# Kernel tuning notes

Hardware: AMD Instinct MI355X
Metric: run time of the kernel (lower is better)

## Reference

```python
import jax, jax.numpy as jnp
import numpy as np

UNITS = 1024
LEVELS = 16
CHUNK = UNITS // LEVELS  # 64


def cumsoftmax(x, mode):
    # softmax then cumsum along last axis; 'r2l' reverses before/after
    if mode == 'l2r':
        return jnp.cumsum(jax.nn.softmax(x, axis=-1), axis=-1)
    else:  # 'r2l'
        xr = x[..., ::-1]
        return jnp.cumsum(jax.nn.softmax(xr, axis=-1), axis=-1)[..., ::-1]


def setup_inputs() -> dict:
    key = jax.random.key(0)
    k1, k2, k3 = jax.random.split(key, 3)
    B, T, D = 32, 512, 1024
    G = UNITS * 4 + LEVELS * 2  # 4128
    x = jax.random.normal(k1, (B, T, D), dtype=jnp.float32)
    kernel = jax.random.normal(k2, (D, G), dtype=jnp.float32) * (1.0 / np.sqrt(D))
    recurrent_kernel = jax.random.normal(k3, (UNITS, G), dtype=jnp.float32) * (1.0 / np.sqrt(UNITS))
    bias = jnp.zeros((G,), dtype=jnp.float32)
    return {"x": x, "kernel": kernel, "recurrent_kernel": recurrent_kernel, "bias": bias}


def reference(x, kernel, recurrent_kernel, bias):
    B, T, D = x.shape
    L, U, C = LEVELS, UNITS, CHUNK

    def one_step(carry, x_t):
        c_last, h_last = carry  # [B, U] each
        z = x_t @ kernel + h_last @ recurrent_kernel + bias  # [B, 4U+2L]
        f_master = cumsoftmax(z[:, :L], 'l2r')[:, :, None]       # [B, L, 1]
        i_master = cumsoftmax(z[:, L:2 * L], 'r2l')[:, :, None]  # [B, L, 1]
        g = z[:, 2 * L:].reshape(B, 4 * L, C)
        f_gate = jax.nn.sigmoid(g[:, :L])
        i_gate = jax.nn.sigmoid(g[:, L:2 * L])
        o_gate = jax.nn.sigmoid(g[:, 2 * L:3 * L])
        c_in = jnp.tanh(g[:, 3 * L:])
        c_prev = c_last.reshape(B, L, C)
        overlap = f_master * i_master
        c_out = (overlap * (f_gate * c_prev + i_gate * c_in)
                 + (f_master - overlap) * c_prev
                 + (i_master - overlap) * c_in)
        h_out = (o_gate * jnp.tanh(c_out)).reshape(B, U)
        c_out = c_out.reshape(B, U)
        return (c_out, h_out), h_out

    init = (jnp.zeros((B, U), x.dtype), jnp.zeros((B, U), x.dtype))
    _, h_seq = jax.lax.scan(one_step, init, jnp.swapaxes(x, 0, 1))  # [T, B, U]
    return jnp.swapaxes(h_seq, 0, 1)  # [B, T, U] (return_sequences=True)
```

## Files before the change

### kernel.cpp

```cpp
#include <hip/hip_runtime.h>

#define TT 512
#define GG 4128
#define GPAD 4224
#define NGATE 64
#define NMST 4
#define NBLK (NGATE + NMST)
#define NTHR 512

typedef _Float16 f16;
typedef _Float16 half8 __attribute__((ext_vector_type(8)));
typedef _Float16 half4 __attribute__((ext_vector_type(4)));
typedef float f32x4 __attribute__((ext_vector_type(4)));
typedef unsigned long long ull;

__device__ __forceinline__ half8 h8(uint4 v) {
  union { uint4 u; half8 h; } c; c.u = v; return c.h;
}

__global__ void k_transpose_cvt(const float* __restrict__ in, f16* __restrict__ out,
                                int R, int C) {
  __shared__ float tile[32][33];
  int bx = blockIdx.x * 32, by = blockIdx.y * 32;
  int tx = threadIdx.x & 31, ty = threadIdx.x >> 5;
#pragma unroll
  for (int j = 0; j < 4; ++j) {
    int r = by + ty + j * 8;
    tile[ty + j * 8][tx] = in[(long)r * C + bx + tx];
  }
  __syncthreads();
#pragma unroll
  for (int j = 0; j < 4; ++j) {
    int c = bx + ty + j * 8;
    out[(long)c * R + by + tx] = (f16)tile[tx][ty + j * 8];
  }
}

__global__ __launch_bounds__(256) void k_gemm_xw(
    const float* __restrict__ X,
    const f16* __restrict__ Bt,
    const float* __restrict__ bias,
    f16* __restrict__ Zm,
    f16* __restrict__ Zg) {
  __shared__ f16 As[128 * 32];
  __shared__ f16 Bs[128 * 32];
  const int m0 = blockIdx.x * 128;
  const int n0 = blockIdx.y * 128;
  const int tid = threadIdx.x;
  const int wave = tid >> 6, lane = tid & 63;
  const int mrow = (wave & 1) * 64, ncol = (wave >> 1) * 64;
  f32x4 acc[4][4];
#pragma unroll
  for (int i = 0; i < 4; ++i)
#pragma unroll
    for (int j = 0; j < 4; ++j)
      acc[i][j] = (f32x4){0.f, 0.f, 0.f, 0.f};

  float4 ra[4];
  uint4 rb[2];
  auto load_tiles = [&](int k0) {
#pragma unroll
    for (int q = 0; q < 4; ++q) {
      int flat = q * 256 + tid;
      int r = flat >> 3, s = flat & 7;
      ra[q] = *(const float4*)(X + (long)(m0 + r) * 1024 + k0 + s * 4);
    }
#pragma unroll
    for (int q = 0; q < 2; ++q) {
      int flat = q * 256 + tid;
      int r = flat >> 2, s = flat & 3;
      rb[q] = *(const uint4*)(Bt + (long)(n0 + r) * 1024 + k0 + s * 8);
    }
  };
  load_tiles(0);
  for (int kt = 0; kt < 32; ++kt) {
    __syncthreads();
#pragma unroll
    for (int q = 0; q < 4; ++q) {
      int flat = q * 256 + tid;
      half4 h;
      h[0] = (f16)ra[q].x; h[1] = (f16)ra[q].y;
      h[2] = (f16)ra[q].z; h[3] = (f16)ra[q].w;
      *(half4*)((char*)As + flat * 8) = h;
    }
#pragma unroll
    for (int q = 0; q < 2; ++q) {
      int flat = q * 256 + tid;
      *(uint4*)((char*)Bs + flat * 16) = rb[q];
    }
    __syncthreads();
    if (kt + 1 < 32) load_tiles((kt + 1) * 32);
    const int kseg2 = ((lane >> 4) * 8) * 2;
    half8 af[4], bf[4];
#pragma unroll
    for (int i = 0; i < 4; ++i) {
      int r = mrow + i * 16 + (lane & 15);
      af[i] = *(const half8*)((const char*)As + r * 64 + kseg2);
      int c = ncol + i * 16 + (lane & 15);
      bf[i] = *(const half8*)((const char*)Bs + c * 64 + kseg2);
    }
#pragma unroll
    for (int i = 0; i < 4; ++i)
#pragma unroll
      for (int j = 0; j < 4; ++j)
        acc[i][j] = __builtin_amdgcn_mfma_f32_16x16x32_f16(af[i], bf[j], acc[i][j], 0, 0, 0);
  }
#pragma unroll
  for (int j = 0; j < 4; ++j) {
    int n = n0 + ncol + j * 16 + (lane & 15);
    if (n < GG) {
      float bv = bias[n];
      const int isM = (n < 32);
      int q = 0, u4 = 0, g2 = 0;
      if (!isM) {
        int k = n - 32;
        q = k >> 10;
        int u = k & 1023;
        g2 = u >> 4;
        u4 = u & 15;
      }
#pragma unroll
      for (int i = 0; i < 4; ++i) {
#pragma unroll
        for (int r = 0; r < 4; ++r) {
          int m = m0 + mrow + i * 16 + (lane >> 4) * 4 + r;
          int b = m >> 9, tt2 = m & 511;
          f16 v = (f16)(acc[i][j][r] + bv);
          if (isM)
            Zm[((long)(tt2 * 32 + b)) * 32 + n] = v;
          else
            Zg[((((long)tt2 * 64 + g2) * 32 + b) * 16 + u4) * 4 + q] = v;
        }
      }
    }
  }
}

__device__ __forceinline__ float sigm(float x) { return 1.f / (1.f + __expf(-x)); }
__device__ __forceinline__ float tanh_(float x) {
  float ax = fabsf(x);
  float e = __expf(-2.f * ax);
  float t = (1.f - e) / (1.f + e);
  return copysignf(t, x);
}
#define AG_LD(p) __hip_atomic_load((p), __ATOMIC_RELAXED, __HIP_MEMORY_SCOPE_AGENT)
#define AG_ST(p, v) __hip_atomic_store((p), (v), __ATOMIC_RELAXED, __HIP_MEMORY_SCOPE_AGENT)

__device__ __forceinline__ void bar_lds() {
  asm volatile("s_waitcnt lgkmcnt(0)" ::: "memory");
  __builtin_amdgcn_sched_barrier(0);
  __builtin_amdgcn_s_barrier();
}

__global__ __launch_bounds__(NTHR, 2) void k_onlstm(
    const f16* __restrict__ Zm, const f16* __restrict__ Zg,
    const f16* __restrict__ Rt, unsigned* __restrict__ hbuf,
    float* __restrict__ cumbuf, unsigned* __restrict__ flags,
    unsigned* __restrict__ mflags, float* __restrict__ Y) {
  extern __shared__ char lds[];
  const int g = blockIdx.x, tid = threadIdx.x;
  const int wave = tid >> 6, lane = tid & 63;
  const int lr = lane & 15, lq = lane >> 4;

  if (g < NGATE) {
    const int kq = wave;
    const int b = tid >> 4;
    const int u = tid & 15;
    const int L0 = g >> 2;
    uint4 bq[16];
    {
      const f16* base = Rt + (long)kq * 128 + lq * 8;
#pragma unroll
      for (int q = 0; q < 4; ++q)
#pragma unroll
        for (int ks = 0; ks < 4; ++ks)
          bq[q * 4 + ks] = *(const uint4*)(base + (long)(32 + q * 1024 + g * 16 + lr) * 1024 + ks * 32);
#pragma unroll
      for (int i = 0; i < 16; ++i)
        asm volatile("" : "+v"(bq[i].x), "+v"(bq[i].y), "+v"(bq[i].z), "+v"(bq[i].w));
    }
    float creg = 0.f;

    for (int t = 0; t < TT; ++t) {
      if (t > 0) {
        for (;;) {
          unsigned v = AG_LD(flags + lane * 16);
          if (__all((int)(v >= (unsigned)t))) break;
        }
      }
      half4 zxh = *(const half4*)(Zg + ((((long)t * 64 + g) * 32 + b) * 16 + u) * 4);
      const ull* hrd = (const ull*)hbuf + (t & 1) * 8192;
      ull hv[16];
#pragma unroll
      for (int it = 0; it < 16; ++it)
        hv[it] = AG_LD(hrd + it * 512 + tid);
      __builtin_amdgcn_sched_barrier(0);
#pragma unroll
      for (int it = 0; it < 16; ++it) {
        int idx = it * 512 + tid;
        int bb = idx >> 8, j8 = idx & 255;
        *(ull*)(lds + ((bb * 128 + ((j8 >> 1) ^ (bb & 7))) << 4) + (j8 & 1) * 8) = hv[it];
      }
      bar_lds();
      f32x4 acc[4][2];
#pragma unroll
      for (int q = 0; q < 4; ++q) {
        acc[q][0] = (f32x4){0.f, 0.f, 0.f, 0.f};
        acc[q][1] = (f32x4){0.f, 0.f, 0.f, 0.f};
      }
#pragma unroll
      for (int ks = 0; ks < 4; ++ks) {
        int ch = kq * 16 + ks * 4 + lq;
        half8 a0 = *(const half8*)(lds + ((lr * 128 + (ch ^ (lr & 7))) << 4));
        half8 a1 = *(const half8*)(lds + (((16 + lr) * 128 + (ch ^ ((16 + lr) & 7))) << 4));
#pragma unroll
        for (int q = 0; q < 4; ++q) {
          acc[q][0] = __builtin_amdgcn_mfma_f32_16x16x32_f16(a0, h8(bq[q * 4 + ks]), acc[q][0], 0, 0, 0);
          acc[q][1] = __builtin_amdgcn_mfma_f32_16x16x32_f16(a1, h8(bq[q * 4 + ks]), acc[q][1], 0, 0, 0);
        }
      }
#pragma unroll
      for (int q = 0; q < 4; ++q)
#pragma unroll
        for (int bt = 0; bt < 2; ++bt) {
          int bsw = (bt * 16 + lq * 4) ^ ((lr & 7) << 2);
          *(f32x4*)(lds + 65536 + (((kq * 64 + q * 16 + lr) * 32 + bsw) << 2)) = acc[q][bt];
        }
      bar_lds();
      for (;;) {
        unsigned v = AG_LD(mflags + (lane & 3) * 16);
        if (__all((int)(v >= (unsigned)(t + 1)))) break;
      }
      unsigned fmu = AG_LD((unsigned*)cumbuf + b * 32 + L0);
      unsigned imu = AG_LD((unsigned*)cumbuf + b * 32 + 16 + L0);
      float z[4];
#pragma unroll
      for (int q = 0; q < 4; ++q) {
        float s = 0.f;
        int bsw = b ^ ((u & 7) << 2);
#pragma unroll
        for (int k8 = 0; k8 < 8; ++k8)
          s += *(const float*)(lds + 65536 + (((k8 * 64 + q * 16 + u) * 32 + bsw) << 2));
        z[q] = s + (float)zxh[q];
      }
      float f = sigm(z[0]), i_ = sigm(z[1]), o = sigm(z[2]);
      float ci = tanh_(z[3]);
      float fm = __uint_as_float(fmu), im = __uint_as_float(imu);
      float ov = fm * im;
      float cn = ov * (f * creg + i_ * ci) + (fm - ov) * creg + (im - ov) * ci;
      creg = cn;
      float hval = o * tanh_(cn);
      float hp = __shfl_xor(hval, 1);
      if (!(u & 1)) {
        union { f16 h[2]; unsigned w; } pk;
        pk.h[0] = (f16)hval;
        pk.h[1] = (f16)hp;
        AG_ST(hbuf + ((t + 1) & 1) * 16384 + b * 512 + g * 8 + (u >> 1), pk.w);
      }
      asm volatile("s_waitcnt vmcnt(0)" ::: "memory");
      __builtin_amdgcn_s_barrier();
      if (tid == 0) AG_ST(flags + g * 16, (unsigned)(t + 1));
      Y[((long)b * TT + t) * 1024 + g * 16 + u] = hval;
    }
  } else {
    const int mid = g - NGATE;
    const int ct = wave & 1, kq4 = wave >> 1;
    const int colm = ct * 16 + lr;
    uint4 bm[8];
    {
      const f16* pm = Rt + (long)colm * 1024 + kq4 * 256 + lq * 8;
#pragma unroll
      for (int ks = 0; ks < 8; ++ks) bm[ks] = *(const uint4*)(pm + ks * 32);
#pragma unroll
      for (int i = 0; i < 8; ++i)
        asm volatile("" : "+v"(bm[i].x), "+v"(bm[i].y), "+v"(bm[i].z), "+v"(bm[i].w));
    }
    const int rb_ = tid & 31, rc = tid >> 5;
    const int sb = tid >> 4, sl = tid & 15;
    float* zpm = (float*)(lds + 65536);
    float* zr = (float*)(lds + 65536 + 16384);

    for (int t = 0; t < TT; ++t) {
      if (t > 0) {
        for (;;) {
          unsigned v = AG_LD(flags + lane * 16);
          if (__all((int)(v >= (unsigned)t))) break;
        }
      }
      f16 zm0 = Zm[((long)t * 32 + rb_) * 32 + rc];
      f16 zm1 = Zm[((long)t * 32 + rb_) * 32 + rc + 16];
      const ull* hrd = (const ull*)hbuf + (t & 1) * 8192;
      ull hv[16];
#pragma unroll
      for (int it = 0; it < 16; ++it)
        hv[it] = AG_LD(hrd + it * 512 + tid);
      __builtin_amdgcn_sched_barrier(0);
#pragma unroll
      for (int it = 0; it < 16; ++it) {
        int idx = it * 512 + tid;
        int bb = idx >> 8, j8 = idx & 255;
        *(ull*)(lds + ((bb * 128 + ((j8 >> 1) ^ (bb & 7))) << 4) + (j8 & 1) * 8) = hv[it];
      }
      bar_lds();
      f32x4 am0 = (f32x4){0.f, 0.f, 0.f, 0.f}, am1 = am0;
#pragma unroll
      for (int ks = 0; ks < 8; ++ks) {
        int ch = kq4 * 32 + ks * 4 + lq;
        half8 a0 = *(const half8*)(lds + ((lr * 128 + (ch ^ (lr & 7))) << 4));
        half8 a1 = *(const half8*)(lds + (((16 + lr) * 128 + (ch ^ ((16 + lr) & 7))) << 4));
        am0 = __builtin_amdgcn_mfma_f32_16x16x32_f16(a0, h8(bm[ks]), am0, 0, 0, 0);
        am1 = __builtin_amdgcn_mfma_f32_16x16x32_f16(a1, h8(bm[ks]), am1, 0, 0, 0);
      }
      {
        int bsw0 = (lq * 4) ^ ((colm & 7) << 2);
        int bsw1 = (16 + lq * 4) ^ ((colm & 7) << 2);
        *(f32x4*)((char*)zpm + (((kq4 * 32 + colm) * 32 + bsw0) << 2)) = am0;
        *(f32x4*)((char*)zpm + (((kq4 * 32 + colm) * 32 + bsw1) << 2)) = am1;
      }
      bar_lds();
#pragma unroll
      for (int rep = 0; rep < 2; ++rep) {
        int c = rc + rep * 16;
        int bsw = rb_ ^ ((c & 7) << 2);
        float s = 0.f;
#pragma unroll
        for (int k4 = 0; k4 < 4; ++k4) s += zpm[(k4 * 32 + c) * 32 + bsw];
        s += (float)(rep ? zm1 : zm0);
        zr[c * 32 + bsw] = s;
      }
      bar_lds();
      float vf[16], vi[16];
#pragma unroll
      for (int j = 0; j < 16; ++j) {
        vf[j] = zr[j * 32 + (sb ^ ((j & 7) << 2))];
        vi[j] = zr[(j + 16) * 32 + (sb ^ ((j & 7) << 2))];
      }
      float mf = vf[0], mi = vi[0];
#pragma unroll
      for (int j = 1; j < 16; ++j) { mf = fmaxf(mf, vf[j]); mi = fmaxf(mi, vi[j]); }
      float sf = 0.f, pf = 0.f, si = 0.f, pi = 0.f;
#pragma unroll
      for (int j = 0; j < 16; ++j) {
        float ef = __expf(vf[j] - mf);
        sf += ef;
        if (j <= sl) pf += ef;
        float ei = __expf(vi[j] - mi);
        si += ei;
        if (j >= sl) pi += ei;
      }
      if ((sb >> 3) == mid) {
        AG_ST((unsigned*)cumbuf + sb * 32 + sl, __float_as_uint(pf / sf));
        AG_ST((unsigned*)cumbuf + sb * 32 + 16 + sl, __float_as_uint(pi / si));
      }
      asm volatile("s_waitcnt vmcnt(0)" ::: "memory");
      __builtin_amdgcn_s_barrier();
      if (tid == 0) AG_ST(mflags + mid * 16, (unsigned)(t + 1));
    }
  }
}

extern "C" void kernel_launch(void* const* d_in, const int* in_sizes, int n_in,
                              void* d_out, int out_size, void* d_ws, size_t ws_size,
                              hipStream_t stream) {
  const float* X = (const float*)d_in[0];
  const float* W = (const float*)d_in[1];
  const float* Rm = (const float*)d_in[2];
  const float* bias = (const float*)d_in[3];
  float* Y = (float*)d_out;
  char* ws = (char*)d_ws;

  const size_t off_flags = 0;
  const size_t off_mflags = 4096;
  const size_t off_cum = 8192;
  const size_t off_h = 16384;
  const size_t off_Zm = 147456;
  const size_t off_Wt = 1196032;
  const size_t off_Rt = 9846784;
  const size_t off_Zg = 18300928;
  const size_t need = off_Zg + (size_t)TT * 64 * 32 * 16 * 4 * 2;
  if (ws_size < need) return;

  unsigned* flags = (unsigned*)(ws + off_flags);
  unsigned* mflags = (unsigned*)(ws + off_mflags);
  float* cumbuf = (float*)(ws + off_cum);
  unsigned* hbuf = (unsigned*)(ws + off_h);
  f16* Zm = (f16*)(ws + off_Zm);
  f16* Wt = (f16*)(ws + off_Wt);
  f16* Rt = (f16*)(ws + off_Rt);
  f16* Zg = (f16*)(ws + off_Zg);

  hipMemsetAsync(ws, 0, off_h + 131072, stream);
  hipMemsetAsync(ws + off_Wt + (size_t)GG * 1024 * 2, 0, (size_t)(GPAD - GG) * 1024 * 2, stream);

  k_transpose_cvt<<<dim3(129, 32), 256, 0, stream>>>(W, Wt, 1024, GG);
  k_transpose_cvt<<<dim3(129, 32), 256, 0, stream>>>(Rm, Rt, 1024, GG);
  k_gemm_xw<<<dim3(128, 33), 256, 0, stream>>>(X, Wt, bias, Zm, Zg);

  hipFuncSetAttribute((const void*)k_onlstm, hipFuncAttributeMaxDynamicSharedMemorySize, 131072);
  k_onlstm<<<NBLK, NTHR, 131072, stream>>>(Zm, Zg, Rt, hbuf, cumbuf, flags, mflags, Y);
}
```

Before: 3.669 ms.

## Compute master cumsoftmax redundantly in every gate block, drop master blocks

Removes the 4 dedicated master-gate blocks and their second global flag handshake. Each of the 64 gate blocks now also runs the 32 master columns of the recurrent matmul on its own. Wave 0 does the cumsoftmax for its own level and shares the result through LDS. This takes one cross-block synchronisation round trip (the mflags spin and cumbuf reads) off every timestep's critical path. In exchange every block does extra MFMA work, holds more weight registers and adds a third LDS barrier per step.

```diff
diff --git a/kernel.cpp b/kernel.cpp
--- a/kernel.cpp
+++ b/kernel.cpp
@@ -3,10 +3,8 @@
 #define TT 512
 #define GG 4128
 #define GPAD 4224
-#define NGATE 64
-#define NMST 4
-#define NBLK (NGATE + NMST)
-#define NTHR 512
+#define NBLK2 64
+#define NTHR2 512
 
 typedef _Float16 f16;
 typedef _Float16 half8 __attribute__((ext_vector_type(8)));
@@ -150,212 +148,171 @@
   asm volatile("s_waitcnt lgkmcnt(0)" ::: "memory");
   __builtin_amdgcn_sched_barrier(0);
   __builtin_amdgcn_s_barrier();
-}
-
-__global__ __launch_bounds__(NTHR, 2) void k_onlstm(
+  __builtin_amdgcn_sched_barrier(0);
+}
+
+__global__ __launch_bounds__(NTHR2, 2) void k_onlstm(
     const f16* __restrict__ Zm, const f16* __restrict__ Zg,
     const f16* __restrict__ Rt, unsigned* __restrict__ hbuf,
-    float* __restrict__ cumbuf, unsigned* __restrict__ flags,
-    unsigned* __restrict__ mflags, float* __restrict__ Y) {
+    unsigned* __restrict__ flags, float* __restrict__ Y) {
   extern __shared__ char lds[];
+  float* cumlds = (float*)(lds + 32768);
   const int g = blockIdx.x, tid = threadIdx.x;
   const int wave = tid >> 6, lane = tid & 63;
   const int lr = lane & 15, lq = lane >> 4;
-
-  if (g < NGATE) {
-    const int kq = wave;
-    const int b = tid >> 4;
-    const int u = tid & 15;
-    const int L0 = g >> 2;
-    uint4 bq[16];
-    {
-      const f16* base = Rt + (long)kq * 128 + lq * 8;
-#pragma unroll
-      for (int q = 0; q < 4; ++q)
-#pragma unroll
-        for (int ks = 0; ks < 4; ++ks)
-          bq[q * 4 + ks] = *(const uint4*)(base + (long)(32 + q * 1024 + g * 16 + lr) * 1024 + ks * 32);
-#pragma unroll
-      for (int i = 0; i < 16; ++i)
-        asm volatile("" : "+v"(bq[i].x), "+v"(bq[i].y), "+v"(bq[i].z), "+v"(bq[i].w));
-    }
-    float creg = 0.f;
-
-    for (int t = 0; t < TT; ++t) {
-      if (t > 0) {
-        for (;;) {
-          unsigned v = AG_LD(flags + lane * 16);
-          if (__all((int)(v >= (unsigned)t))) break;
-        }
-      }
-      half4 zxh = *(const half4*)(Zg + ((((long)t * 64 + g) * 32 + b) * 16 + u) * 4);
-      const ull* hrd = (const ull*)hbuf + (t & 1) * 8192;
-      ull hv[16];
-#pragma unroll
-      for (int it = 0; it < 16; ++it)
-        hv[it] = AG_LD(hrd + it * 512 + tid);
-      __builtin_amdgcn_sched_barrier(0);
-#pragma unroll
-      for (int it = 0; it < 16; ++it) {
-        int idx = it * 512 + tid;
-        int bb = idx >> 8, j8 = idx & 255;
-        *(ull*)(lds + ((bb * 128 + ((j8 >> 1) ^ (bb & 7))) << 4) + (j8 & 1) * 8) = hv[it];
-      }
-      bar_lds();
-      f32x4 acc[4][2];
+  const int kq = wave;
+  const int b = tid >> 4;
+  const int u = tid & 15;
+  const int L0 = g >> 2;
+  const int side = tid >> 5, mb = tid & 31;
+
+  uint4 bq[16], bm[8];
+  {
+    const f16* base = Rt + (long)kq * 128 + lq * 8;
+#pragma unroll
+    for (int q = 0; q < 4; ++q)
+#pragma unroll
+      for (int ks = 0; ks < 4; ++ks)
+        bq[q * 4 + ks] = *(const uint4*)(base + (long)(32 + q * 1024 + g * 16 + lr) * 1024 + ks * 32);
+#pragma unroll
+    for (int ct = 0; ct < 2; ++ct)
+#pragma unroll
+      for (int ks = 0; ks < 4; ++ks)
+        bm[ct * 4 + ks] = *(const uint4*)(base + (long)(ct * 16 + lr) * 1024 + ks * 32);
+#pragma unroll
+    for (int i = 0; i < 16; ++i)
+      asm volatile("" : "+v"(bq[i].x), "+v"(bq[i].y), "+v"(bq[i].z), "+v"(bq[i].w));
+#pragma unroll
+    for (int i = 0; i < 8; ++i)
+      asm volatile("" : "+v"(bm[i].x), "+v"(bm[i].y), "+v"(bm[i].z), "+v"(bm[i].w));
+  }
+  float creg = 0.f;
+
+  for (int t = 0; t < TT; ++t) {
+    half4 zxh = *(const half4*)(Zg + ((((long)t * 64 + g) * 32 + b) * 16 + u) * 4);
+    half8 zmr0, zmr1;
+    if (wave == 0) {
+      const half8* zmp = (const half8*)(Zm + ((long)t * 32 + mb) * 32 + side * 16);
+      zmr0 = zmp[0];
+      zmr1 = zmp[1];
+    }
+    if (t > 0) {
+      for (;;) {
+        unsigned v = AG_LD(flags + lane * 16);
+        if (__all((int)(v >= (unsigned)t))) break;
+      }
+    }
+    const ull* hrd = (const ull*)hbuf + (t & 1) * 8192;
+    ull hv[16];
+#pragma unroll
+    for (int it = 0; it < 16; ++it)
+      hv[it] = AG_LD(hrd + it * 512 + tid);
+    __builtin_amdgcn_sched_barrier(0);
+#pragma unroll
+    for (int it = 0; it < 16; ++it) {
+      int idx = it * 512 + tid;
+      int bb = idx >> 8, j8 = idx & 255;
+      *(ull*)(lds + ((bb * 128 + ((j8 >> 1) ^ (bb & 7))) << 4) + (j8 & 1) * 8) = hv[it];
+    }
+    bar_lds();
+    f32x4 acc[4][2], accm[2][2];
+#pragma unroll
+    for (int q = 0; q < 4; ++q) {
+      acc[q][0] = (f32x4){0.f, 0.f, 0.f, 0.f};
+      acc[q][1] = (f32x4){0.f, 0.f, 0.f, 0.f};
+    }
+#pragma unroll
+    for (int ct = 0; ct < 2; ++ct) {
+      accm[ct][0] = (f32x4){0.f, 0.f, 0.f, 0.f};
+      accm[ct][1] = (f32x4){0.f, 0.f, 0.f, 0.f};
+    }
+#pragma unroll
+    for (int ks = 0; ks < 4; ++ks) {
+      int ch = kq * 16 + ks * 4 + lq;
+      half8 a0 = *(const half8*)(lds + ((lr * 128 + (ch ^ (lr & 7))) << 4));
+      half8 a1 = *(const half8*)(lds + (((16 + lr) * 128 + (ch ^ ((16 + lr) & 7))) << 4));
 #pragma unroll
       for (int q = 0; q < 4; ++q) {
-        acc[q][0] = (f32x4){0.f, 0.f, 0.f, 0.f};
-        acc[q][1] = (f32x4){0.f, 0.f, 0.f, 0.f};
-      }
-#pragma unroll
-      for (int ks = 0; ks < 4; ++ks) {
-        int ch = kq * 16 + ks * 4 + lq;
-        half8 a0 = *(const half8*)(lds + ((lr * 128 + (ch ^ (lr & 7))) << 4));
-        half8 a1 = *(const half8*)(lds + (((16 + lr) * 128 + (ch ^ ((16 + lr) & 7))) << 4));
-#pragma unroll
-        for (int q = 0; q < 4; ++q) {
-          acc[q][0] = __builtin_amdgcn_mfma_f32_16x16x32_f16(a0, h8(bq[q * 4 + ks]), acc[q][0], 0, 0, 0);
-          acc[q][1] = __builtin_amdgcn_mfma_f32_16x16x32_f16(a1, h8(bq[q * 4 + ks]), acc[q][1], 0, 0, 0);
-        }
-      }
-#pragma unroll
-      for (int q = 0; q < 4; ++q)
-#pragma unroll
-        for (int bt = 0; bt < 2; ++bt) {
-          int bsw = (bt * 16 + lq * 4) ^ ((lr & 7) << 2);
-          *(f32x4*)(lds + 65536 + (((kq * 64 + q * 16 + lr) * 32 + bsw) << 2)) = acc[q][bt];
-        }
-      bar_lds();
-      for (;;) {
-        unsigned v = AG_LD(mflags + (lane & 3) * 16);
-        if (__all((int)(v >= (unsigned)(t + 1)))) break;
-      }
-      unsigned fmu = AG_LD((unsigned*)cumbuf + b * 32 + L0);
-      unsigned imu = AG_LD((unsigned*)cumbuf + b * 32 + 16 + L0);
-      float z[4];
-#pragma unroll
-      for (int q = 0; q < 4; ++q) {
+        acc[q][0] = __builtin_amdgcn_mfma_f32_16x16x32_f16(a0, h8(bq[q * 4 + ks]), acc[q][0], 0, 0, 0);
+        acc[q][1] = __builtin_amdgcn_mfma_f32_16x16x32_f16(a1, h8(bq[q * 4 + ks]), acc[q][1], 0, 0, 0);
+      }
+#pragma unroll
+      for (int ct = 0; ct < 2; ++ct) {
+        accm[ct][0] = __builtin_amdgcn_mfma_f32_16x16x32_f16(a0, h8(bm[ct * 4 + ks]), accm[ct][0], 0, 0, 0);
+        accm[ct][1] = __builtin_amdgcn_mfma_f32_16x16x32_f16(a1, h8(bm[ct * 4 + ks]), accm[ct][1], 0, 0, 0);
+      }
+    }
+#pragma unroll
+    for (int q = 0; q < 4; ++q)
+#pragma unroll
+      for (int bt = 0; bt < 2; ++bt) {
+        int bsw = (bt * 16 + lq * 4) ^ ((lr & 7) << 2);
+        *(f32x4*)(lds + 65536 + (((kq * 64 + q * 16 + lr) * 32 + bsw) << 2)) = acc[q][bt];
+      }
+    bar_lds();
+#pragma unroll
+    for (int ct = 0; ct < 2; ++ct)
+#pragma unroll
+      for (int bt = 0; bt < 2; ++bt) {
+        int col = ct * 16 + lr;
+        int bsw = (bt * 16 + lq * 4) ^ ((col & 7) << 2);
+        *(f32x4*)(lds + (((kq * 32 + col) * 32 + bsw) << 2)) = accm[ct][bt];
+      }
+    float z[4];
+#pragma unroll
+    for (int q = 0; q < 4; ++q) {
+      float s = 0.f;
+      int bsw = b ^ ((u & 7) << 2);
+#pragma unroll
+      for (int k8 = 0; k8 < 8; ++k8)
+        s += *(const float*)(lds + 65536 + (((k8 * 64 + q * 16 + u) * 32 + bsw) << 2));
+      z[q] = s + (float)zxh[q];
+    }
+    float f = sigm(z[0]), i_ = sigm(z[1]), o = sigm(z[2]);
+    float ci = tanh_(z[3]);
+    bar_lds();
+    if (wave == 0) {
+      float v[16];
+#pragma unroll
+      for (int j = 0; j < 16; ++j) {
+        int col = side * 16 + j;
+        int bsw = mb ^ ((col & 7) << 2);
         float s = 0.f;
-        int bsw = b ^ ((u & 7) << 2);
 #pragma unroll
         for (int k8 = 0; k8 < 8; ++k8)
-          s += *(const float*)(lds + 65536 + (((k8 * 64 + q * 16 + u) * 32 + bsw) << 2));
-        z[q] = s + (float)zxh[q];
-      }
-      float f = sigm(z[0]), i_ = sigm(z[1]), o = sigm(z[2]);
-      float ci = tanh_(z[3]);
-      float fm = __uint_as_float(fmu), im = __uint_as_float(imu);
-      float ov = fm * im;
-      float cn = ov * (f * creg + i_ * ci) + (fm - ov) * creg + (im - ov) * ci;
-      creg = cn;
-      float hval = o * tanh_(cn);
-      float hp = __shfl_xor(hval, 1);
-      if (!(u & 1)) {
-        union { f16 h[2]; unsigned w; } pk;
-        pk.h[0] = (f16)hval;
-        pk.h[1] = (f16)hp;
-        AG_ST(hbuf + ((t + 1) & 1) * 16384 + b * 512 + g * 8 + (u >> 1), pk.w);
-      }
-      asm volatile("s_waitcnt vmcnt(0)" ::: "memory");
-      __builtin_amdgcn_s_barrier();
-      if (tid == 0) AG_ST(flags + g * 16, (unsigned)(t + 1));
-      Y[((long)b * TT + t) * 1024 + g * 16 + u] = hval;
-    }
-  } else {
-    const int mid = g - NGATE;
-    const int ct = wave & 1, kq4 = wave >> 1;
-    const int colm = ct * 16 + lr;
-    uint4 bm[8];
-    {
-      const f16* pm = Rt + (long)colm * 1024 + kq4 * 256 + lq * 8;
-#pragma unroll
-      for (int ks = 0; ks < 8; ++ks) bm[ks] = *(const uint4*)(pm + ks * 32);
-#pragma unroll
-      for (int i = 0; i < 8; ++i)
-        asm volatile("" : "+v"(bm[i].x), "+v"(bm[i].y), "+v"(bm[i].z), "+v"(bm[i].w));
-    }
-    const int rb_ = tid & 31, rc = tid >> 5;
-    const int sb = tid >> 4, sl = tid & 15;
-    float* zpm = (float*)(lds + 65536);
-    float* zr = (float*)(lds + 65536 + 16384);
-
-    for (int t = 0; t < TT; ++t) {
-      if (t > 0) {
-        for (;;) {
-          unsigned v = AG_LD(flags + lane * 16);
-          if (__all((int)(v >= (unsigned)t))) break;
-        }
-      }
-      f16 zm0 = Zm[((long)t * 32 + rb_) * 32 + rc];
-      f16 zm1 = Zm[((long)t * 32 + rb_) * 32 + rc + 16];
-      const ull* hrd = (const ull*)hbuf + (t & 1) * 8192;
-      ull hv[16];
-#pragma unroll
-      for (int it = 0; it < 16; ++it)
-        hv[it] = AG_LD(hrd + it * 512 + tid);
-      __builtin_amdgcn_sched_barrier(0);
-#pragma unroll
-      for (int it = 0; it < 16; ++it) {
-        int idx = it * 512 + tid;
-        int bb = idx >> 8, j8 = idx & 255;
-        *(ull*)(lds + ((bb * 128 + ((j8 >> 1) ^ (bb & 7))) << 4) + (j8 & 1) * 8) = hv[it];
-      }
-      bar_lds();
-      f32x4 am0 = (f32x4){0.f, 0.f, 0.f, 0.f}, am1 = am0;
-#pragma unroll
-      for (int ks = 0; ks < 8; ++ks) {
-        int ch = kq4 * 32 + ks * 4 + lq;
-        half8 a0 = *(const half8*)(lds + ((lr * 128 + (ch ^ (lr & 7))) << 4));
-        half8 a1 = *(const half8*)(lds + (((16 + lr) * 128 + (ch ^ ((16 + lr) & 7))) << 4));
-        am0 = __builtin_amdgcn_mfma_f32_16x16x32_f16(a0, h8(bm[ks]), am0, 0, 0, 0);
-        am1 = __builtin_amdgcn_mfma_f32_16x16x32_f16(a1, h8(bm[ks]), am1, 0, 0, 0);
-      }
-      {
-        int bsw0 = (lq * 4) ^ ((colm & 7) << 2);
-        int bsw1 = (16 + lq * 4) ^ ((colm & 7) << 2);
-        *(f32x4*)((char*)zpm + (((kq4 * 32 + colm) * 32 + bsw0) << 2)) = am0;
-        *(f32x4*)((char*)zpm + (((kq4 * 32 + colm) * 32 + bsw1) << 2)) = am1;
-      }
-      bar_lds();
-#pragma unroll
-      for (int rep = 0; rep < 2; ++rep) {
-        int c = rc + rep * 16;
-        int bsw = rb_ ^ ((c & 7) << 2);
-        float s = 0.f;
-#pragma unroll
-        for (int k4 = 0; k4 < 4; ++k4) s += zpm[(k4 * 32 + c) * 32 + bsw];
-        s += (float)(rep ? zm1 : zm0);
-        zr[c * 32 + bsw] = s;
-      }
-      bar_lds();
-      float vf[16], vi[16];
+          s += *(const float*)(lds + (((k8 * 32 + col) * 32 + bsw) << 2));
+        v[j] = s + (float)((j < 8) ? zmr0[j] : zmr1[j - 8]);
+      }
+      float mx = v[0];
+#pragma unroll
+      for (int j = 1; j < 16; ++j) mx = fmaxf(mx, v[j]);
+      float ssum = 0.f, p = 0.f;
 #pragma unroll
       for (int j = 0; j < 16; ++j) {
-        vf[j] = zr[j * 32 + (sb ^ ((j & 7) << 2))];
-        vi[j] = zr[(j + 16) * 32 + (sb ^ ((j & 7) << 2))];
-      }
-      float mf = vf[0], mi = vi[0];
-#pragma unroll
-      for (int j = 1; j < 16; ++j) { mf = fmaxf(mf, vf[j]); mi = fmaxf(mi, vi[j]); }
-      float sf = 0.f, pf = 0.f, si = 0.f, pi = 0.f;
-#pragma unroll
-      for (int j = 0; j < 16; ++j) {
-        float ef = __expf(vf[j] - mf);
-        sf += ef;
-        if (j <= sl) pf += ef;
-        float ei = __expf(vi[j] - mi);
-        si += ei;
-        if (j >= sl) pi += ei;
-      }
-      if ((sb >> 3) == mid) {
-        AG_ST((unsigned*)cumbuf + sb * 32 + sl, __float_as_uint(pf / sf));
-        AG_ST((unsigned*)cumbuf + sb * 32 + 16 + sl, __float_as_uint(pi / si));
-      }
-      asm volatile("s_waitcnt vmcnt(0)" ::: "memory");
-      __builtin_amdgcn_s_barrier();
-      if (tid == 0) AG_ST(mflags + mid * 16, (unsigned)(t + 1));
-    }
+        float e = __expf(v[j] - mx);
+        ssum += e;
+        bool take = side ? (j >= L0) : (j <= L0);
+        if (take) p += e;
+      }
+      cumlds[side * 32 + mb] = p / ssum;
+    }
+    bar_lds();
+    float fm = cumlds[b], im = cumlds[32 + b];
+    float ov = fm * im;
+    float cn = ov * (f * creg + i_ * ci) + (fm - ov) * creg + (im - ov) * ci;
+    creg = cn;
+    float hval = o * tanh_(cn);
+    float hp = __shfl_xor(hval, 1);
+    if (!(u & 1)) {
+      union { f16 h[2]; unsigned w; } pk;
+      pk.h[0] = (f16)hval;
+      pk.h[1] = (f16)hp;
+      AG_ST(hbuf + ((t + 1) & 1) * 16384 + b * 512 + g * 8 + (u >> 1), pk.w);
+    }
+    asm volatile("s_waitcnt vmcnt(0)" ::: "memory");
+    __builtin_amdgcn_s_barrier();
+    if (tid == 0) AG_ST(flags + g * 16, (unsigned)(t + 1));
+    Y[((long)b * TT + t) * 1024 + g * 16 + u] = hval;
   }
 }
 
@@ -370,26 +327,22 @@
   char* ws = (char*)d_ws;
 
   const size_t off_flags = 0;
-  const size_t off_mflags = 4096;
-  const size_t off_cum = 8192;
-  const size_t off_h = 16384;
-  const size_t off_Zm = 147456;
-  const size_t off_Wt = 1196032;
-  const size_t off_Rt = 9846784;
-  const size_t off_Zg = 18300928;
+  const size_t off_h = 4096;
+  const size_t off_Zm = 135168;
+  const size_t off_Wt = 1183744;
+  const size_t off_Rt = 9834496;
+  const size_t off_Zg = 18288640;
   const size_t need = off_Zg + (size_t)TT * 64 * 32 * 16 * 4 * 2;
   if (ws_size < need) return;
 
   unsigned* flags = (unsigned*)(ws + off_flags);
-  unsigned* mflags = (unsigned*)(ws + off_mflags);
-  float* cumbuf = (float*)(ws + off_cum);
   unsigned* hbuf = (unsigned*)(ws + off_h);
   f16* Zm = (f16*)(ws + off_Zm);
   f16* Wt = (f16*)(ws + off_Wt);
   f16* Rt = (f16*)(ws + off_Rt);
   f16* Zg = (f16*)(ws + off_Zg);
 
-  hipMemsetAsync(ws, 0, off_h + 131072, stream);
+  hipMemsetAsync(ws, 0, 135168, stream);
   hipMemsetAsync(ws + off_Wt + (size_t)GG * 1024 * 2, 0, (size_t)(GPAD - GG) * 1024 * 2, stream);
 
   k_transpose_cvt<<<dim3(129, 32), 256, 0, stream>>>(W, Wt, 1024, GG);
@@ -397,5 +350,5 @@
   k_gemm_xw<<<dim3(128, 33), 256, 0, stream>>>(X, Wt, bias, Zm, Zg);
 
   hipFuncSetAttribute((const void*)k_onlstm, hipFuncAttributeMaxDynamicSharedMemorySize, 131072);
-  k_onlstm<<<NBLK, NTHR, 131072, stream>>>(Zm, Zg, Rt, hbuf, cumbuf, flags, mflags, Y);
-}
+  k_onlstm<<<NBLK2, NTHR2, 131072, stream>>>(Zm, Zg, Rt, hbuf, flags, Y);
+}
```

After: 4.204 ms. +14.6%, slower.
